# Kernel tuning notes

Hardware: AMD Instinct MI355X
Metric: run time of the kernel (lower is better)

Reference implementation:

```python
import jax, jax.numpy as jnp
import numpy as np

B, N, D = 4, 2048, 512
OUT, H = 512, 8
HD = OUT // H

def setup_inputs() -> dict:
    key = jax.random.key(0)
    ks = jax.random.split(key, 10)
    s = 1.0 / np.sqrt(D)
    x = jax.random.normal(ks[0], (B, N, D), dtype=jnp.float32)
    adj = jax.random.randint(ks[1], (N, N), 0, 2, dtype=jnp.int32)
    Wq = jax.random.uniform(ks[2], (D, OUT), jnp.float32, -s, s)
    bq = jax.random.uniform(ks[3], (OUT,), jnp.float32, -s, s)
    Wk = jax.random.uniform(ks[4], (D, OUT), jnp.float32, -s, s)
    bk = jax.random.uniform(ks[5], (OUT,), jnp.float32, -s, s)
    Wv = jax.random.uniform(ks[6], (D, OUT), jnp.float32, -s, s)
    bv = jax.random.uniform(ks[7], (OUT,), jnp.float32, -s, s)
    so = 1.0 / np.sqrt(OUT)
    Wo = jax.random.uniform(ks[8], (OUT, OUT), jnp.float32, -so, so)
    bo = jax.random.uniform(ks[9], (OUT,), jnp.float32, -so, so)
    return {"x": x, "adj": adj, "Wq": Wq, "bq": bq, "Wk": Wk, "bk": bk,
            "Wv": Wv, "bv": bv, "Wo": Wo, "bo": bo}

def reference(x, adj, Wq, bq, Wk, bk, Wv, bv, Wo, bo):
    scale = HD ** -0.5
    # [B,N,OUT] -> [B,H,N,HD]
    def split_heads(t):
        return t.reshape(B, N, H, HD).transpose(0, 2, 1, 3)
    q = split_heads(x @ Wq + bq)
    k = split_heads(x @ Wk + bk)
    v = split_heads(x @ Wv + bv)
    attn = jnp.einsum('bhnd,bhmd->bhnm', q, k) * scale  # [B,H,N,N]
    mask = (adj == 0)[None, None, :, :]
    attn = jnp.where(mask, jnp.float32(-1e9), attn)
    attn = jax.nn.softmax(attn, axis=-1)
    out = jnp.einsum('bhnm,bhmd->bhnd', attn, v)
    out = out.transpose(0, 2, 1, 3).reshape(B, N, OUT)
    return out @ Wo + bo
```

## Files before the change

### kernel.cpp

```cpp
#include <hip/hip_runtime.h>
#include <math.h>

#define NB   4
#define NN   2048
#define DD   512
#define NOUT 512
#define NH   8
#define HDIM 64

typedef __attribute__((ext_vector_type(4))) short bf16x4;
typedef __attribute__((ext_vector_type(8))) short bf16x8;
typedef __attribute__((ext_vector_type(4))) float f32x4;
#define MFMA32(a, b, c)  __builtin_amdgcn_mfma_f32_16x16x32_bf16(a, b, c, 0, 0, 0)

typedef const __attribute__((address_space(1))) unsigned int* gas_ptr;
typedef __attribute__((address_space(3))) unsigned int* las_ptr;

#define SCALE2 0.18033688f


__device__ inline unsigned short f2bf(float f) {
    unsigned int u = __float_as_uint(f);
    u += 0x7fffu + ((u >> 16) & 1u);
    return (unsigned short)(u >> 16);
}

__device__ inline unsigned int pack_trunc(float lo, float hi) {
    return __builtin_amdgcn_perm(__float_as_uint(hi), __float_as_uint(lo), 0x07060302u);
}

__global__ __launch_bounds__(256) void prep(
    const float* __restrict__ x, unsigned short* __restrict__ xt,
    const float* __restrict__ W0, const float* __restrict__ W1,
    const float* __restrict__ W2, const float* __restrict__ W3,
    unsigned short* __restrict__ Tqkv, unsigned short* __restrict__ To,
    const int* __restrict__ adj, unsigned int* __restrict__ amaskW)
{
    const int blk = blockIdx.x;
    const int t   = threadIdx.x;

    if (blk < 2048) {
        const int i = (blk * 256 + t) * 8;
        const int m = i >> 9, k = i & 511;
        float4 a = *(const float4*)(x + i);
        float4 b = *(const float4*)(x + i + 4);
        ushort4 u0, u1;
        u0.x = f2bf(a.x); u0.y = f2bf(a.y); u0.z = f2bf(a.z); u0.w = f2bf(a.w);
        u1.x = f2bf(b.x); u1.y = f2bf(b.y); u1.z = f2bf(b.z); u1.w = f2bf(b.w);
        unsigned short* dst = xt + ((size_t)(m >> 7) * 65536)
                                 + (k >> 5) * 4096 + (m & 127) * 32 + (k & 31);
        *(ushort4*)dst       = u0;
        *(ushort4*)(dst + 4) = u1;
        return;
    }
    if (blk < 2304) {
        __shared__ float tile[64][65];
        const int idx = blk - 2048;
        const int z = idx >> 6, rem = idx & 63;
        const float* W;
        switch (z) {
            case 0:  W = W0; break;
            case 1:  W = W1; break;
            case 2:  W = W2; break;
            default: W = W3; break;
        }
        unsigned short* T = (z < 3) ? Tqkv : To;
        const int ngbase  = (z < 3) ? z * 512 : 0;
        const int k0 = (rem & 7) * 64, n0 = (rem >> 3) * 64;
        const int r = t >> 6, c = t & 63;
#pragma unroll
        for (int rep = 0; rep < 16; ++rep) {
            const int row = rep * 4 + r;
            tile[row][c] = W[(size_t)(k0 + row) * NOUT + n0 + c];
        }
        __syncthreads();
        const int k  = k0 + c;
        const int ks = k >> 5, kk = k & 31;
#pragma unroll
        for (int rep = 0; rep < 16; ++rep) {
            const int row = rep * 4 + r;
            const int ng  = ngbase + n0 + row;
            T[((size_t)(ng >> 7) * 65536) + ks * 4096 + (ng & 127) * 32 + kk]
                = f2bf(tile[c][row]);
        }
        return;
    }
    {
        const int gid  = (blk - 2304) * 256 + t;
        const int w0   = gid * 4;
        const int qrow = w0 >> 10;
        const int wloc = w0 & 1023;
        const int kb0  = wloc * 2;
        int4 a0 = *(const int4*)(adj + (size_t)qrow * NN + kb0);
        int4 a1 = *(const int4*)(adj + (size_t)qrow * NN + kb0 + 4);
        uint4 m;
        m.x = (a0.x ? 0xFFFFu : 0u) | (a0.y ? 0xFFFF0000u : 0u);
        m.y = (a0.z ? 0xFFFFu : 0u) | (a0.w ? 0xFFFF0000u : 0u);
        m.z = (a1.x ? 0xFFFFu : 0u) | (a1.y ? 0xFFFF0000u : 0u);
        m.w = (a1.z ? 0xFFFFu : 0u) | (a1.w ? 0xFFFF0000u : 0u);
        *(uint4*)(amaskW + (size_t)qrow * 1024 + wloc) = m;
    }
}

#define GT_SETUP(Atil, Wtil)                                                   \
    const int t = threadIdx.x, wave = t >> 6, lane = t & 63;                   \
    const int quad = lane >> 4, l16 = lane & 15;                               \
    const int n0 = blockIdx.x * 128, m0 = blockIdx.y * 128;                    \
    const int wm = (wave & 1) * 64, wn = (wave >> 1) * 64;                     \
    const unsigned short* aP[4];                                               \
    const unsigned short* bP[4];                                               \
    _Pragma("unroll")                                                          \
    for (int mt = 0; mt < 4; ++mt)                                             \
        aP[mt] = Atil + (size_t)blockIdx.y * 65536                             \
               + (wm + mt * 16 + l16) * 32 + quad * 8;                         \
    _Pragma("unroll")                                                          \
    for (int nt = 0; nt < 4; ++nt)                                             \
        bP[nt] = Wtil + (size_t)blockIdx.x * 65536                             \
               + (wn + nt * 16 + l16) * 32 + quad * 8;

#define GT_LOADF(Af, Bf, NTC, ks)                                              \
    _Pragma("unroll")                                                          \
    for (int mt = 0; mt < 4; ++mt) Af[mt] = *(const bf16x8*)(aP[mt] + (ks) * 4096); \
    _Pragma("unroll")                                                          \
    for (int nt = 0; nt < NTC; ++nt) Bf[nt] = *(const bf16x8*)(bP[nt] + (ks) * 4096);

#define GT_MFMA(Af, Bf, NTC)                                                   \
    _Pragma("unroll")                                                          \
    for (int mt = 0; mt < 4; ++mt)                                             \
        _Pragma("unroll")                                                      \
        for (int nt = 0; nt < NTC; ++nt)                                       \
            acc[mt][nt] = MFMA32(Af[mt], Bf[nt], acc[mt][nt]);

#define GT_LOOP(NTC)                                                           \
    f32x4 acc[4][NTC];                                                         \
    _Pragma("unroll")                                                          \
    for (int mt = 0; mt < 4; ++mt)                                             \
        _Pragma("unroll")                                                      \
        for (int nt = 0; nt < NTC; ++nt) acc[mt][nt] = (f32x4){0.f, 0.f, 0.f, 0.f}; \
    bf16x8 aA[4], bA[NTC], aB[4], bB[NTC];                                     \
    GT_LOADF(aA, bA, NTC, 0);                                                  \
    for (int kk = 0; kk < 8; ++kk) {                                           \
        GT_LOADF(aB, bB, NTC, 2 * kk + 1);                                     \
        GT_MFMA(aA, bA, NTC);                                                  \
        if (kk < 7) { GT_LOADF(aA, bA, NTC, 2 * kk + 2); }                     \
        GT_MFMA(aB, bB, NTC);                                                  \
    }

__global__ __launch_bounds__(256, 3) void gemm_qkv(
    const unsigned short* __restrict__ Atil,
    const unsigned short* __restrict__ Wtil,
    const float* __restrict__ bq, const float* __restrict__ bk,
    const float* __restrict__ bv,
    unsigned short* __restrict__ qo, unsigned short* __restrict__ ko,
    unsigned short* __restrict__ vto)
{
    __shared__ unsigned short eps[4 * 2560];
    GT_SETUP(Atil, Wtil);
    GT_LOOP(4);

    const int seg   = n0 >> 9;
    const int nloc0 = n0 & 511;
    const float* bp = (seg == 0) ? bq : (seg == 1) ? bk : bv;
    unsigned short* dst3 = (seg == 0) ? qo : (seg == 1) ? ko : vto;
    const int h = (nloc0 + wn) >> 6;

    float bias4[4];
#pragma unroll
    for (int nt = 0; nt < 4; ++nt) bias4[nt] = bp[nloc0 + wn + nt * 16 + l16];

    unsigned short* Lo = eps + wave * 2560;
#pragma unroll
    for (int mt = 0; mt < 4; ++mt) {
        if (seg < 2) {
#pragma unroll
            for (int nt = 0; nt < 4; ++nt)
#pragma unroll
                for (int r = 0; r < 4; ++r) {
                    float val = acc[mt][nt][r] + bias4[nt];
                    if (seg == 0) val *= SCALE2;
                    Lo[(quad * 4 + r) * 72 + nt * 16 + l16] = f2bf(val);
                }
#pragma unroll
            for (int pass = 0; pass < 2; ++pass) {
                const int row = pass * 8 + (lane >> 3);
                const int mg  = m0 + wm + mt * 16 + row;
                const int bb  = mg >> 11, n = mg & (NN - 1);
                bf16x8 v = *(const bf16x8*)&Lo[row * 72 + (lane & 7) * 8];
                *(bf16x8*)(dst3 + ((size_t)(bb * NH + h) * NN + n) * HDIM
                           + (lane & 7) * 8) = v;
            }
        } else {
#pragma unroll
            for (int nt = 0; nt < 4; ++nt)
#pragma unroll
                for (int r = 0; r < 4; ++r) {
                    const float val = acc[mt][nt][r] + bias4[nt];
                    Lo[(nt * 16 + l16) * 40 + quad * 4 + r] = f2bf(val);
                }
            const int d  = lane;
            const int mg = m0 + wm + mt * 16;
            const int bb = mg >> 11, n = mg & (NN - 1);
            unsigned short* dr = dst3 + ((size_t)(bb * NH + h) * HDIM + d) * NN + n;
            *(bf16x8*)dr       = *(const bf16x8*)&Lo[d * 40];
            *(bf16x8*)(dr + 8) = *(const bf16x8*)&Lo[d * 40 + 8];
        }
    }
}

__global__ __launch_bounds__(256, 3) void gemm_o(
    const unsigned short* __restrict__ Atil,
    const unsigned short* __restrict__ Wtil,
    const float* __restrict__ bias,
    float* __restrict__ C)
{
    const int t = threadIdx.x, wave = t >> 6, lane = t & 63;
    const int quad = lane >> 4, l16 = lane & 15;
    const int n0 = blockIdx.x * 64, m0 = blockIdx.y * 128;
    const int wm = (wave & 1) * 64, wn = (wave >> 1) * 32;
    const unsigned short* aP[4];
    const unsigned short* bP[2];
#pragma unroll
    for (int mt = 0; mt < 4; ++mt)
        aP[mt] = Atil + (size_t)blockIdx.y * 65536
               + (wm + mt * 16 + l16) * 32 + quad * 8;
#pragma unroll
    for (int nt = 0; nt < 2; ++nt)
        bP[nt] = Wtil + (size_t)(n0 >> 7) * 65536
               + ((n0 & 64) + wn + nt * 16 + l16) * 32 + quad * 8;

    GT_LOOP(2);

    float bias2[2];
#pragma unroll
    for (int nt = 0; nt < 2; ++nt) bias2[nt] = bias[n0 + wn + nt * 16 + l16];

#pragma unroll
    for (int mt = 0; mt < 4; ++mt)
#pragma unroll
        for (int nt = 0; nt < 2; ++nt) {
            const int col = n0 + wn + nt * 16 + l16;
#pragma unroll
            for (int r = 0; r < 4; ++r) {
                const int row = m0 + wm + mt * 16 + quad * 4 + r;
                C[(size_t)row * NOUT + col] = acc[mt][nt][r] + bias2[nt];
            }
        }
}

__global__ __launch_bounds__(512) void attn_mfma(
    const unsigned short* __restrict__ qg,
    const unsigned short* __restrict__ kg,
    const unsigned short* __restrict__ vt,
    const unsigned int* __restrict__ amask,
    unsigned short* __restrict__ aot)
{
    __shared__ unsigned short smem[4 * 64 * 64];
    unsigned short* Ka = smem;
    unsigned short* Va = smem + 4096;
    unsigned short* Kb = smem + 8192;
    unsigned short* Vb = smem + 12288;

    const int t    = threadIdx.x;
    const int wave = t >> 6;
    const int lane = t & 63;
    const int quad = lane >> 4;
    const int l16  = lane & 15;

    const int qt = blockIdx.x, h = blockIdx.y, b = blockIdx.z;
    const int bh = b * NH + h;
    const int q0 = qt * 128;

    const unsigned short* kbase  = kg + (size_t)bh * NN * HDIM;
    const unsigned short* vtbase = vt + (size_t)bh * HDIM * NN;

    const int drow = lane >> 3;
    const int dblk = (lane & 7) ^ drow;
    const int p  = wave * 8 + drow;
    const int Lp = (p & 32) + ((p >> 2) & 3) * 8 + ((p >> 4) & 1) * 4 + (p & 3);

    const int sw  = l16 & 7;
    const int bo0 = (quad ^ sw) * 8;
    const int bo1 = bo0 ^ 32;

#define ATT_ISSUE(kt, Kd, Vd)                                                  \
    {                                                                          \
        const int r0 = wave * 8;                                               \
        __builtin_amdgcn_global_load_lds(                                      \
            (gas_ptr)(kbase + (size_t)((kt) * 64 + Lp) * HDIM + dblk * 8),     \
            (las_ptr)(Kd + r0 * 64), 16, 0, 0);                                \
        __builtin_amdgcn_global_load_lds(                                      \
            (gas_ptr)(vtbase + (size_t)(r0 + drow) * NN + (kt) * 64 + dblk * 8), \
            (las_ptr)(Vd + r0 * 64), 16, 0, 0);                                \
    }

    const int myq = q0 + wave * 16 + l16;
    const unsigned short* qrow = qg + ((size_t)bh * NN + myq) * HDIM;
    const bf16x8 bQ0 = *(const bf16x8*)(qrow + quad * 8);
    const bf16x8 bQ1 = *(const bf16x8*)(qrow + quad * 8 + 32);

    const unsigned int* mrow = amask + (size_t)myq * 1024 + quad * 4;
#define MLOAD(kt, c) (*(const uint4*)(mrow + (kt) * 32 + (c) * 16))

    bf16x8 ones8;
#pragma unroll
    for (int j = 0; j < 8; ++j) ones8[j] = (short)0x3F80;

    f32x4 O[4];
#pragma unroll
    for (int dt = 0; dt < 4; ++dt) O[dt] = (f32x4){0.f, 0.f, 0.f, 0.f};
    f32x4 lacc = (f32x4){0.f, 0.f, 0.f, 0.f};

    auto tile = [&](const unsigned short* Ks, const unsigned short* Vs,
                    uint4 mw0, uint4 mw1) {
        bf16x8 Pt[2];
#pragma unroll
        for (int c = 0; c < 2; ++c) {
            const uint4 mw = c ? mw1 : mw0;
            union { unsigned int u[4]; bf16x8 v; } cv;
#pragma unroll
            for (int half = 0; half < 2; ++half) {
                const int nt = c * 2 + half;
                bf16x8 aK0 = *(const bf16x8*)&Ks[(nt * 16 + l16) * 64 + bo0];
                bf16x8 aK1 = *(const bf16x8*)&Ks[(nt * 16 + l16) * 64 + bo1];
                f32x4 s = (f32x4){0.f, 0.f, 0.f, 0.f};
                s = MFMA32(aK0, bQ0, s);
                s = MFMA32(aK1, bQ1, s);
                const float p0 = exp2f(s[0]);
                const float p1 = exp2f(s[1]);
                const float p2 = exp2f(s[2]);
                const float p3 = exp2f(s[3]);
                cv.u[half * 2 + 0] = pack_trunc(p0, p1) & (half ? mw.z : mw.x);
                cv.u[half * 2 + 1] = pack_trunc(p2, p3) & (half ? mw.w : mw.y);
            }
            Pt[c] = cv.v;
            lacc = MFMA32(ones8, Pt[c], lacc);
        }
#pragma unroll
        for (int dt = 0; dt < 4; ++dt)
#pragma unroll
            for (int c = 0; c < 2; ++c) {
                bf16x8 aV = *(const bf16x8*)
                    &Vs[(dt * 16 + l16) * 64 + (((c * 4 + quad) ^ sw) * 8)];
                O[dt] = MFMA32(aV, Pt[c], O[dt]);
            }
    };

    uint4 mA0 = MLOAD(0, 0), mA1 = MLOAD(0, 1);
    uint4 mB0, mB1;
    ATT_ISSUE(0, Ka, Va);
    for (int kk = 0; kk < 16; ++kk) {
        __syncthreads();
        ATT_ISSUE(2 * kk + 1, Kb, Vb);
        mB0 = MLOAD(2 * kk + 1, 0); mB1 = MLOAD(2 * kk + 1, 1);
        tile(Ka, Va, mA0, mA1);
        __syncthreads();
        if (kk < 15) {
            ATT_ISSUE(2 * kk + 2, Ka, Va);
            mA0 = MLOAD(2 * kk + 2, 0); mA1 = MLOAD(2 * kk + 2, 1);
        }
        tile(Kb, Vb, mB0, mB1);
    }
    __syncthreads();

    const float inv = 1.f / lacc[0];
    unsigned short* Lo = smem + wave * (16 * 72);
#pragma unroll
    for (int dt = 0; dt < 4; ++dt) {
        const float v0 = O[dt][0] * inv, v1 = O[dt][1] * inv;
        const float v2 = O[dt][2] * inv, v3 = O[dt][3] * inv;
        *(unsigned int*)&Lo[l16 * 72 + dt * 16 + quad * 4]     = pack_trunc(v0, v1);
        *(unsigned int*)&Lo[l16 * 72 + dt * 16 + quad * 4 + 2] = pack_trunc(v2, v3);
    }
    const int rr = lane >> 2;
    const int qq = q0 + wave * 16 + rr;
    const int m  = b * NN + qq;
    const int mb = m >> 7, r = m & 127;
#pragma unroll
    for (int i = 0; i < 2; ++i) {
        const int ch = (lane & 3) + 4 * i;
        const int ks = h * 2 + (ch >> 2);
        bf16x8 val = *(const bf16x8*)&Lo[rr * 72 + ch * 8];
        *(bf16x8*)(aot + (size_t)mb * 65536 + ks * 4096 + r * 32 + (ch & 3) * 8) = val;
    }
#undef ATT_ISSUE
#undef MLOAD
}

extern "C" void kernel_launch(void* const* d_in, const int* in_sizes, int n_in,
                              void* d_out, int out_size, void* d_ws, size_t ws_size,
                              hipStream_t stream)
{
    const float* x   = (const float*)d_in[0];
    const int*   adj = (const int*)  d_in[1];
    const float* Wq  = (const float*)d_in[2];
    const float* bq  = (const float*)d_in[3];
    const float* Wk  = (const float*)d_in[4];
    const float* bk  = (const float*)d_in[5];
    const float* Wv  = (const float*)d_in[6];
    const float* bv  = (const float*)d_in[7];
    const float* Wo  = (const float*)d_in[8];
    const float* bo  = (const float*)d_in[9];
    float* out = (float*)d_out;

    const size_t qkv_elems = (size_t)NB * NH * NN * HDIM;
    unsigned short* xt    = (unsigned short*)d_ws;
    unsigned short* q     = xt   + qkv_elems;
    unsigned short* kb    = q    + qkv_elems;
    unsigned short* vtb   = kb   + qkv_elems;
    unsigned short* tWqkv = vtb  + qkv_elems;
    unsigned short* tWo   = tWqkv + (size_t)3 * DD * NOUT;
    unsigned int*   amaskW = (unsigned int*)(tWo + (size_t)DD * NOUT);
    unsigned short* aot   = xt;

    prep<<<dim3(4352), 256, 0, stream>>>(x, xt, Wq, Wk, Wv, Wo,
                                         tWqkv, tWo, adj, amaskW);

    gemm_qkv<<<dim3(12, 64), 256, 0, stream>>>(xt, tWqkv, bq, bk, bv, q, kb, vtb);

    attn_mfma<<<dim3(NN / 128, NH, NB), 512, 0, stream>>>(q, kb, vtb, amaskW, aot);

    gemm_o<<<dim3(8, 64), 256, 0, stream>>>(aot, tWo, bo, out);
}
```

Measured before the change: 196.2 us.

## Double attention K/V stage depth to two tiles per buffer with MFMA priority

The attention loop now loads two 64-key tiles per double-buffer stage instead of one, doubling LDS to 64KB and halving the number of block-wide barriers. The PV MFMA section is wrapped in s_setprio so waves doing matrix work get issue priority, and launch bounds request 4 waves per EU. The cost is more LDS per block, which may limit how many blocks fit per CU, and more registers held live for the extra mask words.

```diff
diff --git a/kernel.cpp b/kernel.cpp
--- a/kernel.cpp
+++ b/kernel.cpp
@@ -247,18 +247,18 @@
         }
 }
 
-__global__ __launch_bounds__(512) void attn_mfma(
+__global__ __launch_bounds__(512, 4) void attn_mfma(
     const unsigned short* __restrict__ qg,
     const unsigned short* __restrict__ kg,
     const unsigned short* __restrict__ vt,
     const unsigned int* __restrict__ amask,
     unsigned short* __restrict__ aot)
 {
-    __shared__ unsigned short smem[4 * 64 * 64];
+    __shared__ unsigned short smem[4 * 64 * 128];
     unsigned short* Ka = smem;
-    unsigned short* Va = smem + 4096;
-    unsigned short* Kb = smem + 8192;
-    unsigned short* Vb = smem + 12288;
+    unsigned short* Va = smem + 8192;
+    unsigned short* Kb = smem + 16384;
+    unsigned short* Vb = smem + 24576;
 
     const int t    = threadIdx.x;
     const int wave = t >> 6;
@@ -305,6 +305,8 @@
 #pragma unroll
     for (int j = 0; j < 8; ++j) ones8[j] = (short)0x3F80;
 
+    const f32x4 z4 = (f32x4){0.f, 0.f, 0.f, 0.f};
+
     f32x4 O[4];
 #pragma unroll
     for (int dt = 0; dt < 4; ++dt) O[dt] = (f32x4){0.f, 0.f, 0.f, 0.f};
@@ -322,8 +324,7 @@
                 const int nt = c * 2 + half;
                 bf16x8 aK0 = *(const bf16x8*)&Ks[(nt * 16 + l16) * 64 + bo0];
                 bf16x8 aK1 = *(const bf16x8*)&Ks[(nt * 16 + l16) * 64 + bo1];
-                f32x4 s = (f32x4){0.f, 0.f, 0.f, 0.f};
-                s = MFMA32(aK0, bQ0, s);
+                f32x4 s = MFMA32(aK0, bQ0, z4);
                 s = MFMA32(aK1, bQ1, s);
                 const float p0 = exp2f(s[0]);
                 const float p1 = exp2f(s[1]);
@@ -335,6 +336,7 @@
             Pt[c] = cv.v;
             lacc = MFMA32(ones8, Pt[c], lacc);
         }
+        __builtin_amdgcn_s_setprio(1);
 #pragma unroll
         for (int dt = 0; dt < 4; ++dt)
 #pragma unroll
@@ -343,22 +345,31 @@
                     &Vs[(dt * 16 + l16) * 64 + (((c * 4 + quad) ^ sw) * 8)];
                 O[dt] = MFMA32(aV, Pt[c], O[dt]);
             }
+        __builtin_amdgcn_s_setprio(0);
     };
 
     uint4 mA0 = MLOAD(0, 0), mA1 = MLOAD(0, 1);
-    uint4 mB0, mB1;
+    uint4 mA2 = MLOAD(1, 0), mA3 = MLOAD(1, 1);
+    uint4 mB0, mB1, mB2, mB3;
     ATT_ISSUE(0, Ka, Va);
-    for (int kk = 0; kk < 16; ++kk) {
+    ATT_ISSUE(1, Ka + 4096, Va + 4096);
+    for (int it = 0; it < 8; ++it) {
         __syncthreads();
-        ATT_ISSUE(2 * kk + 1, Kb, Vb);
-        mB0 = MLOAD(2 * kk + 1, 0); mB1 = MLOAD(2 * kk + 1, 1);
+        ATT_ISSUE(4 * it + 2, Kb, Vb);
+        ATT_ISSUE(4 * it + 3, Kb + 4096, Vb + 4096);
+        mB0 = MLOAD(4 * it + 2, 0); mB1 = MLOAD(4 * it + 2, 1);
+        mB2 = MLOAD(4 * it + 3, 0); mB3 = MLOAD(4 * it + 3, 1);
         tile(Ka, Va, mA0, mA1);
+        tile(Ka + 4096, Va + 4096, mA2, mA3);
         __syncthreads();
-        if (kk < 15) {
-            ATT_ISSUE(2 * kk + 2, Ka, Va);
-            mA0 = MLOAD(2 * kk + 2, 0); mA1 = MLOAD(2 * kk + 2, 1);
+        if (it < 7) {
+            ATT_ISSUE(4 * it + 4, Ka, Va);
+            ATT_ISSUE(4 * it + 5, Ka + 4096, Va + 4096);
+            mA0 = MLOAD(4 * it + 4, 0); mA1 = MLOAD(4 * it + 4, 1);
+            mA2 = MLOAD(4 * it + 5, 0); mA3 = MLOAD(4 * it + 5, 1);
         }
         tile(Kb, Vb, mB0, mB1);
+        tile(Kb + 4096, Vb + 4096, mB2, mB3);
     }
     __syncthreads();
 
```

Result: slower. 206.4 us (+5.2%).

## Split key tile across wave pairs so each wave handles two query groups

Applied to the files above, without the earlier changes.

The attention kernel now pairs waves: each wave owns 32 queries (two 16-row groups) but only half of each 64-key tile. K and V fragments loaded from LDS are reused across both query groups, which halves LDS reads per MFMA. Partial O and row sums are reduced through shared memory at the end, costing extra LDS space, two more barriers and more registers. Launch bounds now request 4 blocks per CU.

```diff
diff --git a/kernel.cpp b/kernel.cpp
--- a/kernel.cpp
+++ b/kernel.cpp
@@ -247,14 +247,14 @@
         }
 }
 
-__global__ __launch_bounds__(512) void attn_mfma(
+__global__ __launch_bounds__(512, 4) void attn_mfma(
     const unsigned short* __restrict__ qg,
     const unsigned short* __restrict__ kg,
     const unsigned short* __restrict__ vt,
     const unsigned int* __restrict__ amask,
     unsigned short* __restrict__ aot)
 {
-    __shared__ unsigned short smem[4 * 64 * 64];
+    __shared__ unsigned short smem[18432];
     unsigned short* Ka = smem;
     unsigned short* Va = smem + 4096;
     unsigned short* Kb = smem + 8192;
@@ -265,6 +265,8 @@
     const int lane = t & 63;
     const int quad = lane >> 4;
     const int l16  = lane & 15;
+    const int pair = wave >> 1;
+    const int hk   = wave & 1;
 
     const int qt = blockIdx.x, h = blockIdx.y, b = blockIdx.z;
     const int bh = b * NH + h;
@@ -293,56 +295,71 @@
             (las_ptr)(Vd + r0 * 64), 16, 0, 0);                                \
     }
 
-    const int myq = q0 + wave * 16 + l16;
-    const unsigned short* qrow = qg + ((size_t)bh * NN + myq) * HDIM;
-    const bf16x8 bQ0 = *(const bf16x8*)(qrow + quad * 8);
-    const bf16x8 bQ1 = *(const bf16x8*)(qrow + quad * 8 + 32);
-
-    const unsigned int* mrow = amask + (size_t)myq * 1024 + quad * 4;
-#define MLOAD(kt, c) (*(const uint4*)(mrow + (kt) * 32 + (c) * 16))
+    const int myq0 = q0 + pair * 32 + l16;
+    const int myq1 = myq0 + 16;
+    const unsigned short* qrow0 = qg + ((size_t)bh * NN + myq0) * HDIM;
+    const unsigned short* qrow1 = qg + ((size_t)bh * NN + myq1) * HDIM;
+    const bf16x8 bQ0g0 = *(const bf16x8*)(qrow0 + quad * 8);
+    const bf16x8 bQ1g0 = *(const bf16x8*)(qrow0 + quad * 8 + 32);
+    const bf16x8 bQ0g1 = *(const bf16x8*)(qrow1 + quad * 8);
+    const bf16x8 bQ1g1 = *(const bf16x8*)(qrow1 + quad * 8 + 32);
+
+    const unsigned int* mrow0 = amask + (size_t)myq0 * 1024 + quad * 4;
+    const unsigned int* mrow1 = amask + (size_t)myq1 * 1024 + quad * 4;
+#define MLOAD(kt, g) (*(const uint4*)(((g) ? mrow1 : mrow0) + (kt) * 32 + hk * 16))
 
     bf16x8 ones8;
 #pragma unroll
     for (int j = 0; j < 8; ++j) ones8[j] = (short)0x3F80;
 
-    f32x4 O[4];
-#pragma unroll
-    for (int dt = 0; dt < 4; ++dt) O[dt] = (f32x4){0.f, 0.f, 0.f, 0.f};
-    f32x4 lacc = (f32x4){0.f, 0.f, 0.f, 0.f};
+    f32x4 O[4][2];
+#pragma unroll
+    for (int dt = 0; dt < 4; ++dt)
+#pragma unroll
+        for (int g = 0; g < 2; ++g) O[dt][g] = (f32x4){0.f, 0.f, 0.f, 0.f};
+    f32x4 lacc[2];
+    lacc[0] = (f32x4){0.f, 0.f, 0.f, 0.f};
+    lacc[1] = (f32x4){0.f, 0.f, 0.f, 0.f};
 
     auto tile = [&](const unsigned short* Ks, const unsigned short* Vs,
-                    uint4 mw0, uint4 mw1) {
+                    uint4 mwg0, uint4 mwg1) {
+        bf16x8 aK[2][2];
+#pragma unroll
+        for (int kg = 0; kg < 2; ++kg) {
+            const int nt = hk * 2 + kg;
+            aK[kg][0] = *(const bf16x8*)&Ks[(nt * 16 + l16) * 64 + bo0];
+            aK[kg][1] = *(const bf16x8*)&Ks[(nt * 16 + l16) * 64 + bo1];
+        }
         bf16x8 Pt[2];
 #pragma unroll
-        for (int c = 0; c < 2; ++c) {
-            const uint4 mw = c ? mw1 : mw0;
+        for (int g = 0; g < 2; ++g) {
+            const uint4 mw = g ? mwg1 : mwg0;
+            const bf16x8 q0f = g ? bQ0g1 : bQ0g0;
+            const bf16x8 q1f = g ? bQ1g1 : bQ1g0;
             union { unsigned int u[4]; bf16x8 v; } cv;
 #pragma unroll
-            for (int half = 0; half < 2; ++half) {
-                const int nt = c * 2 + half;
-                bf16x8 aK0 = *(const bf16x8*)&Ks[(nt * 16 + l16) * 64 + bo0];
-                bf16x8 aK1 = *(const bf16x8*)&Ks[(nt * 16 + l16) * 64 + bo1];
+            for (int kg = 0; kg < 2; ++kg) {
                 f32x4 s = (f32x4){0.f, 0.f, 0.f, 0.f};
-                s = MFMA32(aK0, bQ0, s);
-                s = MFMA32(aK1, bQ1, s);
+                s = MFMA32(aK[kg][0], q0f, s);
+                s = MFMA32(aK[kg][1], q1f, s);
                 const float p0 = exp2f(s[0]);
                 const float p1 = exp2f(s[1]);
                 const float p2 = exp2f(s[2]);
                 const float p3 = exp2f(s[3]);
-                cv.u[half * 2 + 0] = pack_trunc(p0, p1) & (half ? mw.z : mw.x);
-                cv.u[half * 2 + 1] = pack_trunc(p2, p3) & (half ? mw.w : mw.y);
-            }
-            Pt[c] = cv.v;
-            lacc = MFMA32(ones8, Pt[c], lacc);
-        }
-#pragma unroll
-        for (int dt = 0; dt < 4; ++dt)
-#pragma unroll
-            for (int c = 0; c < 2; ++c) {
-                bf16x8 aV = *(const bf16x8*)
-                    &Vs[(dt * 16 + l16) * 64 + (((c * 4 + quad) ^ sw) * 8)];
-                O[dt] = MFMA32(aV, Pt[c], O[dt]);
-            }
+                cv.u[kg * 2 + 0] = pack_trunc(p0, p1) & (kg ? mw.z : mw.x);
+                cv.u[kg * 2 + 1] = pack_trunc(p2, p3) & (kg ? mw.w : mw.y);
+            }
+            Pt[g] = cv.v;
+            lacc[g] = MFMA32(ones8, Pt[g], lacc[g]);
+        }
+#pragma unroll
+        for (int dt = 0; dt < 4; ++dt) {
+            bf16x8 aV = *(const bf16x8*)
+                &Vs[(dt * 16 + l16) * 64 + (((hk * 4 + quad) ^ sw) * 8)];
+#pragma unroll
+            for (int g = 0; g < 2; ++g)
+                O[dt][g] = MFMA32(aV, Pt[g], O[dt][g]);
+        }
     };
 
     uint4 mA0 = MLOAD(0, 0), mA1 = MLOAD(0, 1);
@@ -362,25 +379,56 @@
     }
     __syncthreads();
 
-    const float inv = 1.f / lacc[0];
-    unsigned short* Lo = smem + wave * (16 * 72);
-#pragma unroll
-    for (int dt = 0; dt < 4; ++dt) {
-        const float v0 = O[dt][0] * inv, v1 = O[dt][1] * inv;
-        const float v2 = O[dt][2] * inv, v3 = O[dt][3] * inv;
-        *(unsigned int*)&Lo[l16 * 72 + dt * 16 + quad * 4]     = pack_trunc(v0, v1);
-        *(unsigned int*)&Lo[l16 * 72 + dt * 16 + quad * 4 + 2] = pack_trunc(v2, v3);
-    }
-    const int rr = lane >> 2;
-    const int qq = q0 + wave * 16 + rr;
-    const int m  = b * NN + qq;
-    const int mb = m >> 7, r = m & 127;
-#pragma unroll
-    for (int i = 0; i < 2; ++i) {
-        const int ch = (lane & 3) + 4 * i;
-        const int ks = h * 2 + (ch >> 2);
-        bf16x8 val = *(const bf16x8*)&Lo[rr * 72 + ch * 8];
-        *(bf16x8*)(aot + (size_t)mb * 65536 + ks * 4096 + r * 32 + (ch & 3) * 8) = val;
+    float* F   = (float*)smem;
+    float* myF = F + ((size_t)pair * 64 + lane) * 36;
+    if (hk == 1) {
+#pragma unroll
+        for (int dt = 0; dt < 4; ++dt)
+#pragma unroll
+            for (int g = 0; g < 2; ++g)
+                *(f32x4*)(myF + dt * 8 + g * 4) = O[dt][g];
+        myF[32] = lacc[0][0];
+        myF[33] = lacc[1][0];
+    }
+    __syncthreads();
+    float inv0 = 0.f, inv1 = 0.f;
+    if (hk == 0) {
+#pragma unroll
+        for (int dt = 0; dt < 4; ++dt)
+#pragma unroll
+            for (int g = 0; g < 2; ++g) {
+                const f32x4 o2 = *(const f32x4*)(myF + dt * 8 + g * 4);
+                O[dt][g] += o2;
+            }
+        inv0 = 1.f / (lacc[0][0] + myF[32]);
+        inv1 = 1.f / (lacc[1][0] + myF[33]);
+    }
+    __syncthreads();
+
+    if (hk == 0) {
+#pragma unroll
+        for (int g = 0; g < 2; ++g) {
+            const float inv = g ? inv1 : inv0;
+            unsigned short* Lo = smem + (pair * 2 + g) * 1152;
+#pragma unroll
+            for (int dt = 0; dt < 4; ++dt) {
+                const float v0 = O[dt][g][0] * inv, v1 = O[dt][g][1] * inv;
+                const float v2 = O[dt][g][2] * inv, v3 = O[dt][g][3] * inv;
+                *(unsigned int*)&Lo[l16 * 72 + dt * 16 + quad * 4]     = pack_trunc(v0, v1);
+                *(unsigned int*)&Lo[l16 * 72 + dt * 16 + quad * 4 + 2] = pack_trunc(v2, v3);
+            }
+            const int rr = lane >> 2;
+            const int qq = q0 + pair * 32 + g * 16 + rr;
+            const int m  = b * NN + qq;
+            const int mb = m >> 7, r = m & 127;
+#pragma unroll
+            for (int i = 0; i < 2; ++i) {
+                const int ch = (lane & 3) + 4 * i;
+                const int ks = h * 2 + (ch >> 2);
+                bf16x8 val = *(const bf16x8*)&Lo[rr * 72 + ch * 8];
+                *(bf16x8*)(aot + (size_t)mb * 65536 + ks * 4096 + r * 32 + (ch & 3) * 8) = val;
+            }
+        }
     }
 #undef ATT_ISSUE
 #undef MLOAD
```

Result: no change. 192.5 us (-1.8%).
